# Kernel tuning notes

Hardware: AMD Instinct MI355X
Metric: run time of the kernel (lower is better)

## Reference

```python
import jax, jax.numpy as jnp
import numpy as np

N, D_IN, D_ATTN, STEPS, TOPK, TAU = 8192, 512, 64, 2, 16, 1.0
LN_EPS = 1e-5


def setup_inputs() -> dict:
    key = jax.random.key(0)
    ks = jax.random.split(key, 6)
    s_in = 1.0 / np.sqrt(D_IN)
    s_at = 1.0 / np.sqrt(D_ATTN)
    return {
        "X": jax.random.normal(ks[0], (N, D_IN), jnp.float32),
        "W1": jax.random.normal(ks[1], (D_ATTN, D_IN), jnp.float32) * s_in,
        "W2": jax.random.normal(ks[2], (D_ATTN, D_ATTN), jnp.float32) * s_at,
        "W3": jax.random.normal(ks[3], (D_ATTN, D_IN), jnp.float32) * s_in,
        "mixW": jax.random.normal(ks[4], (STEPS, D_IN, D_IN), jnp.float32) * s_in,
        "mixB": jax.random.normal(ks[5], (STEPS, D_IN), jnp.float32) * 0.01,
        "gamma": jnp.ones((D_IN,), jnp.float32),
        "beta": jnp.zeros((D_IN,), jnp.float32),
    }


def reference(X, W1, W2, W3, mixW, mixB, gamma, beta):
    # --- adjacency from features (top-k masked attention) ---
    Q = X @ W1.T                    # [N, d_attn]
    K = X @ W3.T                    # [N, d_attn]
    S = (Q @ W2) @ K.T / TAU        # [N, N]  (W2.weight used as raw matrix)
    _, idx = jax.lax.top_k(S, TOPK) # top-k along dim 1, [N, topk]
    mask = jnp.full_like(S, -jnp.inf)
    rows = jnp.arange(N)[:, None]
    mask = mask.at[rows, idx].set(0.0)
    P = jax.nn.softmax(S + mask, axis=1)  # row-sparse (k nonzeros) but dense-stored
    # dropout p=0 (eval mode) -> identity

    # --- iterative message passing with per-step mix ---
    H = X
    Z = jnp.zeros_like(X)
    for n in range(STEPS):  # bidir=False
        H = P @ H
        Z = Z + H @ mixW[n].T + mixB[n]

    # --- residual + LayerNorm ---
    y = X + Z
    mu = jnp.mean(y, axis=-1, keepdims=True)
    var = jnp.mean((y - mu) ** 2, axis=-1, keepdims=True)
    return (y - mu) * jax.lax.rsqrt(var + LN_EPS) * gamma + beta
```

## Files before the change

kernel.cpp:

```cpp
#include <hip/hip_runtime.h>

#define NROWS 8192
#define DIN   512
#define DATT  64
#define KTOP  16
#define CMAX  128
#define SROWS 32
#define NSPLIT 2
#define KSB   256
#define THRC  2.45f
#define NEG_INF (-3.0e38f)

typedef _Float16 f16x8 __attribute__((ext_vector_type(8)));
typedef float    fx4   __attribute__((ext_vector_type(4)));

__device__ __forceinline__ void gload_lds16(const void* g, void* l) {
    __builtin_amdgcn_global_load_lds((const __attribute__((address_space(1))) void*)g,
                                     (__attribute__((address_space(3))) void*)l, 16, 0, 0);
}

__global__ void k_conv_f16(const float* __restrict__ in, _Float16* __restrict__ out, int n) {
    int i = blockIdx.x * 256 + threadIdx.x;
    if (i < n) out[i] = (_Float16)in[i];
}

__global__ void k_split(const float* __restrict__ in, _Float16* __restrict__ hi,
                        _Float16* __restrict__ lo, int n) {
    int i = blockIdx.x * 256 + threadIdx.x;
    if (i < n) {
        float x = in[i];
        _Float16 h = (_Float16)x;
        hi[i] = h;
        lo[i] = (_Float16)(x - (float)h);
    }
}

__global__ void k_wsplit(const float* __restrict__ W1, const float* __restrict__ W2,
                         const float* __restrict__ W3, _Float16* __restrict__ Whi,
                         _Float16* __restrict__ Wlo, int* __restrict__ CandCnt) {
    int id = blockIdx.x * 256 + threadIdx.x;
    if (id < NROWS) CandCnt[id] = 0;
    int c = id >> 9, k = id & 511;
    float r;
    if (c < 64) {
        float acc = 0.f;
        #pragma unroll 8
        for (int e = 0; e < 64; e++) acc += W1[e*512 + k] * W2[e*64 + c];
        r = acc;
    } else {
        r = W3[(c - 64)*512 + k];
    }
    _Float16 h = (_Float16)r;
    Whi[id] = h;
    Wlo[id] = (_Float16)(r - (float)h);
}

__launch_bounds__(256)
__global__ void k_proj(const _Float16* __restrict__ Ahi, const _Float16* __restrict__ Alo,
                       const _Float16* __restrict__ Bhi, const _Float16* __restrict__ Blo,
                       float* __restrict__ Cf, _Float16* __restrict__ Ch) {
    const int tid = threadIdx.x, lane = tid & 63, wid = tid >> 6;
    const int bm = blockIdx.x * 128 + wid * 32;
    const int bn = blockIdx.y * 64;
    const int lr = lane & 15, kg = lane >> 4;

    fx4 acc[2][4];
    #pragma unroll
    for (int m = 0; m < 2; m++)
        #pragma unroll
        for (int n = 0; n < 4; n++) acc[m][n] = (fx4){0.f,0.f,0.f,0.f};

    const _Float16* Aph = Ahi + (size_t)(bm + lr) * DIN + kg*8;
    const _Float16* Apl = Alo + (size_t)(bm + lr) * DIN + kg*8;
    const _Float16* Bph = Bhi + (size_t)(bn + lr) * DIN + kg*8;
    const _Float16* Bpl = Blo + (size_t)(bn + lr) * DIN + kg*8;

    for (int k0 = 0; k0 < DIN; k0 += 32) {
        f16x8 ah[2], al[2], bh[4], bl[4];
        #pragma unroll
        for (int m = 0; m < 2; m++) {
            ah[m] = *(const f16x8*)(Aph + (size_t)m*16*DIN + k0);
            al[m] = *(const f16x8*)(Apl + (size_t)m*16*DIN + k0);
        }
        #pragma unroll
        for (int n = 0; n < 4; n++) {
            bh[n] = *(const f16x8*)(Bph + (size_t)n*16*DIN + k0);
            bl[n] = *(const f16x8*)(Bpl + (size_t)n*16*DIN + k0);
        }
        #pragma unroll
        for (int m = 0; m < 2; m++)
            #pragma unroll
            for (int n = 0; n < 4; n++) {
                acc[m][n] = __builtin_amdgcn_mfma_f32_16x16x32_f16(ah[m], bh[n], acc[m][n], 0,0,0);
                acc[m][n] = __builtin_amdgcn_mfma_f32_16x16x32_f16(ah[m], bl[n], acc[m][n], 0,0,0);
                acc[m][n] = __builtin_amdgcn_mfma_f32_16x16x32_f16(al[m], bh[n], acc[m][n], 0,0,0);
            }
    }

    #pragma unroll
    for (int m = 0; m < 2; m++)
        #pragma unroll
        for (int n = 0; n < 4; n++) {
            const int col = bn + n*16 + lr;
            #pragma unroll
            for (int r = 0; r < 4; r++) {
                const int row = bm + m*16 + kg*4 + r;
                const size_t off = (size_t)row * 128 + col;
                float v = acc[m][n][r];
                Cf[off] = v;
                Ch[off] = (_Float16)v;
            }
        }
}

__launch_bounds__(256)
__global__ void k_kstats1(const float* __restrict__ AK, float* __restrict__ KCp,
                          float* __restrict__ ksp) {
    __shared__ float kr[32][64];
    const int tid = threadIdx.x;
    const int r0  = blockIdx.x * 32;
    #pragma unroll
    for (int q = 0; q < 8; q++) {
        int e = tid + q*256;
        int rr = e >> 6, cc = e & 63;
        kr[rr][cc] = AK[(size_t)(r0 + rr) * 128 + 64 + cc];
    }
    __syncthreads();

    const int i0 = tid >> 2;
    const int j0 = (tid & 3) * 16;
    float acc[16];
    #pragma unroll
    for (int e = 0; e < 16; e++) acc[e] = 0.f;
    #pragma unroll 8
    for (int rr = 0; rr < 32; rr++) {
        const float ki = kr[rr][i0];
        #pragma unroll
        for (int e = 0; e < 16; e++) acc[e] += ki * kr[rr][j0 + e];
    }
    float* o = KCp + (size_t)blockIdx.x * 4096 + i0*64 + j0;
    #pragma unroll
    for (int e = 0; e < 16; e++) o[e] = acc[e];

    if (tid < 64) {
        float s = 0.f;
        #pragma unroll 8
        for (int rr = 0; rr < 32; rr++) s += kr[rr][tid];
        ksp[blockIdx.x*64 + tid] = s;
    }
}

__launch_bounds__(256)
__global__ void k_kstats2(const float* __restrict__ KCp, const float* __restrict__ ksp,
                          float* __restrict__ KC, float* __restrict__ ksum) {
    const int o = blockIdx.x*256 + threadIdx.x;
    float s0=0.f, s1=0.f, s2=0.f, s3=0.f;
    for (int b = 0; b < KSB; b += 4) {
        s0 += KCp[(size_t)b*4096 + o];
        s1 += KCp[(size_t)(b+1)*4096 + o];
        s2 += KCp[(size_t)(b+2)*4096 + o];
        s3 += KCp[(size_t)(b+3)*4096 + o];
    }
    KC[o] = (s0+s1) + (s2+s3);
    if (o < 64) {
        float t0=0.f, t1=0.f;
        for (int b = 0; b < KSB; b += 2) {
            t0 += ksp[b*64 + o];
            t1 += ksp[(b+1)*64 + o];
        }
        ksum[o] = t0 + t1;
    }
}

__launch_bounds__(256)
__global__ void k_thr(const float* __restrict__ AK, const float* __restrict__ ksum,
                      const float* __restrict__ KC, float* __restrict__ Thr) {
    __shared__ float sKC[64*65];
    __shared__ float skb[64];
    const int tid = threadIdx.x, lane = tid & 63, wv = tid >> 6;

    for (int e = tid; e < 4096; e += 256)
        sKC[(e >> 6)*65 + (e & 63)] = KC[e];
    if (tid < 64) skb[tid] = ksum[tid] * (1.f/(float)NROWS);
    __syncthreads();

    #pragma unroll
    for (int j = 0; j < 4; j++) {
        const int row = blockIdx.x*16 + wv*4 + j;
        const float a_l = AK[(size_t)row * 128 + lane];
        float w = 0.f;
        #pragma unroll 16
        for (int d = 0; d < 64; d++) w += sKC[lane*65 + d] * __shfl(a_l, d);
        float p  = a_l * w;
        float mu = a_l * skb[lane];
        #pragma unroll
        for (int off = 1; off < 64; off <<= 1) {
            p  += __shfl_xor(p,  off);
            mu += __shfl_xor(mu, off);
        }
        if (lane == 0) {
            float var = p * (1.f/(float)NROWS) - mu*mu;
            Thr[row] = mu + THRC * sqrtf(fmaxf(var, 0.f));
        }
    }
}

__launch_bounds__(256)
__global__ void k_sfilter(const _Float16* __restrict__ AKh, const float* __restrict__ Thr,
                          int* __restrict__ CandIdx, int* __restrict__ CandCnt) {
    const int tid = threadIdx.x, lane = tid & 63, wid = tid >> 6;
    const int bm = blockIdx.x * SROWS;
    const int lr = lane & 15, kg = lane >> 4;

    __shared__ int scnt[SROWS];
    __shared__ int sbase[SROWS];
    __shared__ int scand[SROWS][CMAX];
    if (tid < SROWS) scnt[tid] = 0;

    f16x8 af[2][2];
    #pragma unroll
    for (int m = 0; m < 2; m++)
        #pragma unroll
        for (int ks = 0; ks < 2; ks++)
            af[m][ks] = *(const f16x8*)(AKh + (size_t)(bm + m*16 + lr)*128 + ks*32 + kg*8);

    float thr[2][4];
    #pragma unroll
    for (int m = 0; m < 2; m++)
        #pragma unroll
        for (int r = 0; r < 4; r++)
            thr[m][r] = Thr[bm + m*16 + kg*4 + r];

    __syncthreads();

    const int c0 = blockIdx.y * (NROWS/NSPLIT) + wid*64;
    f16x8 bf[4][2], bnx[4][2];
    #pragma unroll
    for (int n = 0; n < 4; n++)
        #pragma unroll
        for (int ks = 0; ks < 2; ks++)
            bnx[n][ks] = *(const f16x8*)(AKh + (size_t)(c0 + n*16 + lr)*128 + 64 + ks*32 + kg*8);

    const int NIT = (NROWS/NSPLIT)/256;
    for (int it = 0; it < NIT; ++it) {
        #pragma unroll
        for (int n = 0; n < 4; n++)
            #pragma unroll
            for (int ks = 0; ks < 2; ks++)
                bf[n][ks] = bnx[n][ks];
        const int cbase = c0 + it*256;
        if (it + 1 < NIT) {
            const int cnx = cbase + 256;
            #pragma unroll
            for (int n = 0; n < 4; n++)
                #pragma unroll
                for (int ks = 0; ks < 2; ks++)
                    bnx[n][ks] = *(const f16x8*)(AKh + (size_t)(cnx + n*16 + lr)*128 + 64 + ks*32 + kg*8);
        }

        fx4 acc[2][4];
        #pragma unroll
        for (int m = 0; m < 2; m++)
            #pragma unroll
            for (int n = 0; n < 4; n++) acc[m][n] = (fx4){0.f,0.f,0.f,0.f};
        #pragma unroll
        for (int ks = 0; ks < 2; ks++)
            #pragma unroll
            for (int m = 0; m < 2; m++)
                #pragma unroll
                for (int n = 0; n < 4; n++)
                    acc[m][n] = __builtin_amdgcn_mfma_f32_16x16x32_f16(af[m][ks], bf[n][ks], acc[m][n], 0,0,0);

        #pragma unroll
        for (int m = 0; m < 2; m++) {
            #pragma unroll
            for (int r = 0; r < 4; r++) {
                const int row = m*16 + kg*4 + r;
                const float t = thr[m][r];
                #pragma unroll
                for (int n = 0; n < 4; n++) {
                    const float v = acc[m][n][r];
                    if (v > t) {
                        const int p = atomicAdd(&scnt[row], 1);
                        if (p < CMAX) scand[row][p] = cbase + n*16 + lr;
                    }
                }
            }
        }
    }

    __syncthreads();
    if (tid < SROWS) sbase[tid] = atomicAdd(&CandCnt[bm + tid], min(scnt[tid], CMAX));
    __syncthreads();
    for (int e = tid; e < SROWS*CMAX; e += 256) {
        const int row = e / CMAX, slot = e % CMAX;
        if (slot < min(scnt[row], CMAX)) {
            const int dst = sbase[row] + slot;
            if (dst < CMAX) CandIdx[(size_t)(bm + row)*CMAX + dst] = scand[row][slot];
        }
    }
}

__launch_bounds__(256)
__global__ void k_sel(const float* __restrict__ AK, const int* __restrict__ CandIdx,
                      const int* __restrict__ CandCnt,
                      float* __restrict__ Pval, int* __restrict__ Pidx) {
    const int wv   = threadIdx.x >> 6;
    const int row  = blockIdx.x*4 + wv;
    const int lane = threadIdx.x & 63;
    const int cnt  = min(CandCnt[row], CMAX);

    __shared__ float ss[4][CMAX];
    __shared__ int   sx[4][CMAX];

    const fx4* a4 = (const fx4*)(AK + (size_t)row * 128);

    float sv[2]; int si[2];
    #pragma unroll
    for (int q = 0; q < 2; q++) {
        const int c = lane + q*64;
        if (c < cnt) {
            const int idx = CandIdx[(size_t)row * CMAX + c];
            const fx4* k4 = (const fx4*)(AK + (size_t)idx * 128 + 64);
            float p0 = 0.f, p1 = 0.f, p2 = 0.f, p3 = 0.f;
            #pragma unroll
            for (int d = 0; d < 4; d++) {
                fx4 a0 = a4[d*4+0], k0 = k4[d*4+0];
                fx4 a1 = a4[d*4+1], k1 = k4[d*4+1];
                fx4 a2 = a4[d*4+2], k2 = k4[d*4+2];
                fx4 a3 = a4[d*4+3], k3 = k4[d*4+3];
                p0 += a0[0]*k0[0] + a0[1]*k0[1] + a0[2]*k0[2] + a0[3]*k0[3];
                p1 += a1[0]*k1[0] + a1[1]*k1[1] + a1[2]*k1[2] + a1[3]*k1[3];
                p2 += a2[0]*k2[0] + a2[1]*k2[1] + a2[2]*k2[2] + a2[3]*k2[3];
                p3 += a3[0]*k3[0] + a3[1]*k3[1] + a3[2]*k3[2] + a3[3]*k3[3];
            }
            sv[q] = (p0 + p1) + (p2 + p3); si[q] = idx;
        } else { sv[q] = NEG_INF; si[q] = 0x7fffffff; }
        ss[wv][c] = sv[q];
        sx[wv][c] = si[q];
    }

    float m = fmaxf(sv[0], sv[1]);
    #pragma unroll
    for (int off = 1; off < 64; off <<= 1) m = fmaxf(m, __shfl_xor(m, off));

    int r0 = 0, r1 = 0;
    #pragma unroll 4
    for (int j = 0; j < cnt; j++) {
        const float sj = ss[wv][j];
        const int   ij = sx[wv][j];
        r0 += (sj > sv[0]) || (sj == sv[0] && ij < si[0]);
        r1 += (sj > sv[1]) || (sj == sv[1] && ij < si[1]);
    }

    const float e0 = (lane      < cnt && r0 < KTOP) ? __expf(sv[0] - m) : 0.f;
    const float e1 = (lane + 64 < cnt && r1 < KTOP) ? __expf(sv[1] - m) : 0.f;
    float Z = e0 + e1;
    #pragma unroll
    for (int off = 1; off < 64; off <<= 1) Z += __shfl_xor(Z, off);
    const float rZ = 1.f / Z;

    if (lane < cnt && r0 < KTOP) {
        Pval[(size_t)row*KTOP + r0] = e0 * rZ;
        Pidx[(size_t)row*KTOP + r0] = si[0];
    }
    if (lane + 64 < cnt && r1 < KTOP) {
        Pval[(size_t)row*KTOP + r1] = e1 * rZ;
        Pidx[(size_t)row*KTOP + r1] = si[1];
    }
    if (lane >= cnt && lane < KTOP) {
        Pval[(size_t)row*KTOP + lane] = 0.f;
        Pidx[(size_t)row*KTOP + lane] = row;
    }
}

__launch_bounds__(256)
__global__ void k_gather(const float* __restrict__ Pval, const int* __restrict__ Pidx,
                         const _Float16* __restrict__ Hin, _Float16* __restrict__ Hout) {
    const int wv = threadIdx.x >> 6, lane = threadIdx.x & 63;
    const int row = blockIdx.x*4 + wv;
    const float pvl = Pval[row*KTOP + (lane & 15)];
    const int   pil = Pidx[row*KTOP + (lane & 15)];

    float acc[8];
    #pragma unroll
    for (int j = 0; j < 8; j++) acc[j] = 0.f;
    #pragma unroll
    for (int t = 0; t < KTOP; t++) {
        const float p  = __shfl(pvl, t);
        const int   ix = __shfl(pil, t);
        f16x8 h = *(const f16x8*)(Hin + (size_t)ix*DIN + lane*8);
        #pragma unroll
        for (int j = 0; j < 8; j++) acc[j] += p * (float)h[j];
    }
    f16x8 o;
    #pragma unroll
    for (int j = 0; j < 8; j++) o[j] = (_Float16)acc[j];
    *(f16x8*)(Hout + (size_t)row*DIN + lane*8) = o;
}

template<bool ACCUM>
__launch_bounds__(256)
__global__ void k_gemm_lds(const _Float16* __restrict__ A, const _Float16* __restrict__ B,
                           float* __restrict__ Cf, const float* __restrict__ bias,
                           int M, int N, int K) {
    __shared__ __align__(16) char smem[24576];
    const int tid = threadIdx.x, lane = tid & 63, wid = tid >> 6;
    const int bm = blockIdx.x * 128;
    const int bn = blockIdx.y * 64;
    const int lr = lane & 15, kg = lane >> 4;

    const int srow  = lane >> 3;
    const int scolh = ((lane & 7) ^ srow) * 8;

    fx4 acc[2][4];
    #pragma unroll
    for (int m = 0; m < 2; m++)
        #pragma unroll
        for (int n = 0; n < 4; n++) acc[m][n] = (fx4){0.f,0.f,0.f,0.f};

    const int sw = (lr & 7) << 4;

    for (int k0 = 0; k0 < K; k0 += 64) {
        #pragma unroll
        for (int q = 0; q < 4; q++) {
            const int r = (wid*4 + q)*8 + srow;
            gload_lds16(A + (size_t)(bm + r)*K + k0 + scolh, smem + (wid*4 + q)*1024);
        }
        #pragma unroll
        for (int q = 0; q < 2; q++) {
            const int r = (wid*2 + q)*8 + srow;
            gload_lds16(B + (size_t)(bn + r)*K + k0 + scolh, smem + 16384 + (wid*2 + q)*1024);
        }
        __syncthreads();

        f16x8 af[2][2], bf[4][2];
        #pragma unroll
        for (int m = 0; m < 2; m++) {
            const int arow = wid*32 + m*16 + lr;
            #pragma unroll
            for (int ks = 0; ks < 2; ks++)
                af[m][ks] = *(const f16x8*)(smem + arow*128 + ((ks*64 + kg*16) ^ sw));
        }
        #pragma unroll
        for (int n = 0; n < 4; n++) {
            const int brow = n*16 + lr;
            #pragma unroll
            for (int ks = 0; ks < 2; ks++)
                bf[n][ks] = *(const f16x8*)(smem + 16384 + brow*128 + ((ks*64 + kg*16) ^ sw));
        }
        #pragma unroll
        for (int ks = 0; ks < 2; ks++)
            #pragma unroll
            for (int m = 0; m < 2; m++)
                #pragma unroll
                for (int n = 0; n < 4; n++)
                    acc[m][n] = __builtin_amdgcn_mfma_f32_16x16x32_f16(af[m][ks], bf[n][ks], acc[m][n], 0,0,0);
        __syncthreads();
    }

    #pragma unroll
    for (int m = 0; m < 2; m++) {
        #pragma unroll
        for (int n = 0; n < 4; n++) {
            const int col = bn + n*16 + lr;
            const float bv = bias[col];
            #pragma unroll
            for (int r = 0; r < 4; r++) {
                const int row = bm + wid*32 + m*16 + kg*4 + r;
                const size_t off = (size_t)row * N + col;
                float v = acc[m][n][r] + bv;
                if (ACCUM) v += Cf[off];
                Cf[off] = v;
            }
        }
    }
}

__launch_bounds__(256)
__global__ void k_ln(const float* __restrict__ X, const float* __restrict__ Z,
                     const float* __restrict__ gamma, const float* __restrict__ beta,
                     float* __restrict__ out) {
    const int row = blockIdx.x, tid = threadIdx.x;
    const size_t base = (size_t)row * DIN;
    float y0 = X[base + tid]       + Z[base + tid];
    float y1 = X[base + tid + 256] + Z[base + tid + 256];
    float s  = y0 + y1;
    float s2 = y0*y0 + y1*y1;
    #pragma unroll
    for (int off = 32; off > 0; off >>= 1) {
        s  += __shfl_down(s,  off);
        s2 += __shfl_down(s2, off);
    }
    __shared__ float as_[4], as2_[4], mv[2];
    const int lane = tid & 63, w = tid >> 6;
    if (lane == 0) { as_[w] = s; as2_[w] = s2; }
    __syncthreads();
    if (tid == 0) {
        float ts = as_[0] + as_[1] + as_[2] + as_[3];
        float t2 = as2_[0] + as2_[1] + as2_[2] + as2_[3];
        float mu  = ts / 512.f;
        float var = t2 / 512.f - mu*mu;
        mv[0] = mu; mv[1] = rsqrtf(var + 1e-5f);
    }
    __syncthreads();
    const float mu = mv[0], rs = mv[1];
    out[base + tid]       = (y0 - mu) * rs * gamma[tid]       + beta[tid];
    out[base + tid + 256] = (y1 - mu) * rs * gamma[tid + 256] + beta[tid + 256];
}

extern "C" void kernel_launch(void* const* d_in, const int* in_sizes, int n_in,
                              void* d_out, int out_size, void* d_ws, size_t ws_size,
                              hipStream_t stream) {
    const float* X     = (const float*)d_in[0];
    const float* W1    = (const float*)d_in[1];
    const float* W2    = (const float*)d_in[2];
    const float* W3    = (const float*)d_in[3];
    const float* mixW  = (const float*)d_in[4];
    const float* mixB  = (const float*)d_in[5];
    const float* gamma = (const float*)d_in[6];
    const float* beta  = (const float*)d_in[7];
    float* out = (float*)d_out;

    char* ws = (char*)d_ws;
    size_t off = 0;
    auto alloc = [&](size_t bytes) {
        void* p = ws + off;
        off += (bytes + 255) & ~(size_t)255;
        return p;
    };
    _Float16* Xhi  = (_Float16*)alloc((size_t)NROWS*DIN*2);
    _Float16* Xlo  = (_Float16*)alloc((size_t)NROWS*DIN*2);
    _Float16* Whi  = (_Float16*)alloc((size_t)128*DIN*2);
    _Float16* Wlo  = (_Float16*)alloc((size_t)128*DIN*2);
    float*    Af32 = (float*)alloc((size_t)NROWS*128*4);
    _Float16* AKh  = (_Float16*)alloc((size_t)NROWS*128*2);
    _Float16* mWh  = (_Float16*)alloc((size_t)2*DIN*DIN*2);
    float*    KCp  = (float*)alloc((size_t)KSB*4096*4);
    float*    ksp  = (float*)alloc((size_t)KSB*64*4);
    float*    ksum = (float*)alloc(64*4);
    float*    KC   = (float*)alloc(4096*4);
    float*    Thr  = (float*)alloc((size_t)NROWS*4);
    float*    Pval = (float*)alloc((size_t)NROWS*KTOP*4);
    int*      Pidx = (int*)alloc((size_t)NROWS*KTOP*4);
    int*      CandIdx = (int*)alloc((size_t)NROWS*CMAX*4);
    int*      CandCnt = (int*)alloc((size_t)NROWS*4);
    _Float16* H1h  = (_Float16*)alloc((size_t)NROWS*DIN*2);
    _Float16* H2h  = (_Float16*)alloc((size_t)NROWS*DIN*2);
    float*    Zacc = (float*)alloc((size_t)NROWS*DIN*4);
    (void)ws_size; (void)in_sizes; (void)n_in; (void)out_size;

    dim3 b256(256);

    k_wsplit<<<dim3(128*DIN/256), b256, 0, stream>>>(W1, W2, W3, Whi, Wlo, CandCnt);
    k_split<<<dim3(NROWS*DIN/256), b256, 0, stream>>>(X, Xhi, Xlo, NROWS*DIN);
    k_conv_f16<<<dim3(2*DIN*DIN/256), b256, 0, stream>>>(mixW, mWh, 2*DIN*DIN);

    k_proj<<<dim3(NROWS/128, 2), b256, 0, stream>>>(Xhi, Xlo, Whi, Wlo, Af32, AKh);

    k_kstats1<<<dim3(KSB), b256, 0, stream>>>(Af32, KCp, ksp);
    k_kstats2<<<dim3(16), b256, 0, stream>>>(KCp, ksp, KC, ksum);
    k_thr<<<dim3(NROWS/16), b256, 0, stream>>>(Af32, ksum, KC, Thr);

    k_sfilter<<<dim3(NROWS/SROWS, NSPLIT), b256, 0, stream>>>(AKh, Thr, CandIdx, CandCnt);

    k_sel<<<dim3(NROWS/4), b256, 0, stream>>>(Af32, CandIdx, CandCnt, Pval, Pidx);

    k_gather<<<dim3(NROWS/4), b256, 0, stream>>>(Pval, Pidx, Xhi, H1h);
    k_gemm_lds<false><<<dim3(NROWS/128, DIN/64), b256, 0, stream>>>(
        H1h, mWh, Zacc, mixB, NROWS, DIN, DIN);
    k_gather<<<dim3(NROWS/4), b256, 0, stream>>>(Pval, Pidx, H1h, H2h);
    k_gemm_lds<true><<<dim3(NROWS/128, DIN/64), b256, 0, stream>>>(
        H2h, mWh + (size_t)DIN*DIN, Zacc, mixB + DIN, NROWS, DIN, DIN);
    k_ln<<<dim3(NROWS), b256, 0, stream>>>(X, Zacc, gamma, beta, out);
}
```

Baseline: 285.8 us.

## Fuse X hi/lo split into projection and merge two mix GEMMs into one K=1024 GEMM

Removes the standalone X split and mixW conversion kernels. The projection kernel now reads fp32 X directly, splits it into hi/lo f16 in registers, and writes Xhi from one column block. The two per-step mix GEMMs are concatenated along K into a single GEMM over [H1|H2] with a concatenated weight and summed bias. This avoids the Zacc read-modify-write and an extra launch. NSPLIT for the filter is also raised from 2 to 4; in exchange the projection does more fp32 global reads per block.

```diff
diff --git a/kernel.cpp b/kernel.cpp
--- a/kernel.cpp
+++ b/kernel.cpp
@@ -6,7 +6,7 @@
 #define KTOP  16
 #define CMAX  128
 #define SROWS 32
-#define NSPLIT 2
+#define NSPLIT 4
 #define KSB   256
 #define THRC  2.45f
 #define NEG_INF (-3.0e38f)
@@ -17,22 +17,6 @@
 __device__ __forceinline__ void gload_lds16(const void* g, void* l) {
     __builtin_amdgcn_global_load_lds((const __attribute__((address_space(1))) void*)g,
                                      (__attribute__((address_space(3))) void*)l, 16, 0, 0);
-}
-
-__global__ void k_conv_f16(const float* __restrict__ in, _Float16* __restrict__ out, int n) {
-    int i = blockIdx.x * 256 + threadIdx.x;
-    if (i < n) out[i] = (_Float16)in[i];
-}
-
-__global__ void k_split(const float* __restrict__ in, _Float16* __restrict__ hi,
-                        _Float16* __restrict__ lo, int n) {
-    int i = blockIdx.x * 256 + threadIdx.x;
-    if (i < n) {
-        float x = in[i];
-        _Float16 h = (_Float16)x;
-        hi[i] = h;
-        lo[i] = (_Float16)(x - (float)h);
-    }
 }
 
 __global__ void k_wsplit(const float* __restrict__ W1, const float* __restrict__ W2,
@@ -55,14 +39,24 @@
     Wlo[id] = (_Float16)(r - (float)h);
 }
 
-__launch_bounds__(256)
-__global__ void k_proj(const _Float16* __restrict__ Ahi, const _Float16* __restrict__ Alo,
-                       const _Float16* __restrict__ Bhi, const _Float16* __restrict__ Blo,
-                       float* __restrict__ Cf, _Float16* __restrict__ Ch) {
+__global__ void k_mixprep(const float* __restrict__ mixW, const float* __restrict__ mixB,
+                          _Float16* __restrict__ mWcat, float* __restrict__ biasSum) {
+    int id = blockIdx.x * 256 + threadIdx.x;
+    int j = id >> 10, k = id & 1023;
+    float v = (k < 512) ? mixW[j*512 + k] : mixW[262144 + j*512 + (k - 512)];
+    mWcat[id] = (_Float16)v;
+    if (id < 512) biasSum[id] = mixB[id] + mixB[512 + id];
+}
+
+__launch_bounds__(256)
+__global__ void k_proj(const float* __restrict__ X, const _Float16* __restrict__ Bhi,
+                       const _Float16* __restrict__ Blo, float* __restrict__ Cf,
+                       _Float16* __restrict__ Ch, _Float16* __restrict__ Xhi) {
     const int tid = threadIdx.x, lane = tid & 63, wid = tid >> 6;
     const int bm = blockIdx.x * 128 + wid * 32;
     const int bn = blockIdx.y * 64;
     const int lr = lane & 15, kg = lane >> 4;
+    const bool wx = (blockIdx.y == 0);
 
     fx4 acc[2][4];
     #pragma unroll
@@ -70,8 +64,6 @@
         #pragma unroll
         for (int n = 0; n < 4; n++) acc[m][n] = (fx4){0.f,0.f,0.f,0.f};
 
-    const _Float16* Aph = Ahi + (size_t)(bm + lr) * DIN + kg*8;
-    const _Float16* Apl = Alo + (size_t)(bm + lr) * DIN + kg*8;
     const _Float16* Bph = Bhi + (size_t)(bn + lr) * DIN + kg*8;
     const _Float16* Bpl = Blo + (size_t)(bn + lr) * DIN + kg*8;
 
@@ -79,8 +71,16 @@
         f16x8 ah[2], al[2], bh[4], bl[4];
         #pragma unroll
         for (int m = 0; m < 2; m++) {
-            ah[m] = *(const f16x8*)(Aph + (size_t)m*16*DIN + k0);
-            al[m] = *(const f16x8*)(Apl + (size_t)m*16*DIN + k0);
+            const fx4* xp = (const fx4*)(X + (size_t)(bm + m*16 + lr)*DIN + kg*8 + k0);
+            fx4 x0 = xp[0], x1 = xp[1];
+            #pragma unroll
+            for (int j = 0; j < 4; j++) {
+                _Float16 h0 = (_Float16)x0[j];
+                _Float16 h1 = (_Float16)x1[j];
+                ah[m][j]   = h0; al[m][j]   = (_Float16)(x0[j] - (float)h0);
+                ah[m][j+4] = h1; al[m][j+4] = (_Float16)(x1[j] - (float)h1);
+            }
+            if (wx) *(f16x8*)(Xhi + (size_t)(bm + m*16 + lr)*DIN + kg*8 + k0) = ah[m];
         }
         #pragma unroll
         for (int n = 0; n < 4; n++) {
@@ -399,11 +399,10 @@
     *(f16x8*)(Hout + (size_t)row*DIN + lane*8) = o;
 }
 
-template<bool ACCUM>
-__launch_bounds__(256)
-__global__ void k_gemm_lds(const _Float16* __restrict__ A, const _Float16* __restrict__ B,
-                           float* __restrict__ Cf, const float* __restrict__ bias,
-                           int M, int N, int K) {
+__launch_bounds__(256)
+__global__ void k_gemm_mix(const _Float16* __restrict__ A1, const _Float16* __restrict__ A2,
+                           const _Float16* __restrict__ B, float* __restrict__ Cf,
+                           const float* __restrict__ bias) {
     __shared__ __align__(16) char smem[24576];
     const int tid = threadIdx.x, lane = tid & 63, wid = tid >> 6;
     const int bm = blockIdx.x * 128;
@@ -421,16 +420,18 @@
 
     const int sw = (lr & 7) << 4;
 
-    for (int k0 = 0; k0 < K; k0 += 64) {
+    for (int k0 = 0; k0 < 1024; k0 += 64) {
+        const _Float16* Asrc = (k0 < 512) ? A1 : A2;
+        const int ka = k0 & 511;
         #pragma unroll
         for (int q = 0; q < 4; q++) {
             const int r = (wid*4 + q)*8 + srow;
-            gload_lds16(A + (size_t)(bm + r)*K + k0 + scolh, smem + (wid*4 + q)*1024);
+            gload_lds16(Asrc + (size_t)(bm + r)*DIN + ka + scolh, smem + (wid*4 + q)*1024);
         }
         #pragma unroll
         for (int q = 0; q < 2; q++) {
             const int r = (wid*2 + q)*8 + srow;
-            gload_lds16(B + (size_t)(bn + r)*K + k0 + scolh, smem + 16384 + (wid*2 + q)*1024);
+            gload_lds16(B + (size_t)(bn + r)*1024 + k0 + scolh, smem + 16384 + (wid*2 + q)*1024);
         }
         __syncthreads();
 
@@ -468,10 +469,7 @@
             #pragma unroll
             for (int r = 0; r < 4; r++) {
                 const int row = bm + wid*32 + m*16 + kg*4 + r;
-                const size_t off = (size_t)row * N + col;
-                float v = acc[m][n][r] + bv;
-                if (ACCUM) v += Cf[off];
-                Cf[off] = v;
+                Cf[(size_t)row * DIN + col] = acc[m][n][r] + bv;
             }
         }
     }
@@ -530,12 +528,12 @@
         return p;
     };
     _Float16* Xhi  = (_Float16*)alloc((size_t)NROWS*DIN*2);
-    _Float16* Xlo  = (_Float16*)alloc((size_t)NROWS*DIN*2);
     _Float16* Whi  = (_Float16*)alloc((size_t)128*DIN*2);
     _Float16* Wlo  = (_Float16*)alloc((size_t)128*DIN*2);
     float*    Af32 = (float*)alloc((size_t)NROWS*128*4);
     _Float16* AKh  = (_Float16*)alloc((size_t)NROWS*128*2);
-    _Float16* mWh  = (_Float16*)alloc((size_t)2*DIN*DIN*2);
+    _Float16* mWcat= (_Float16*)alloc((size_t)DIN*1024*2);
+    float*    bSum = (float*)alloc(512*4);
     float*    KCp  = (float*)alloc((size_t)KSB*4096*4);
     float*    ksp  = (float*)alloc((size_t)KSB*64*4);
     float*    ksum = (float*)alloc(64*4);
@@ -553,10 +551,9 @@
     dim3 b256(256);
 
     k_wsplit<<<dim3(128*DIN/256), b256, 0, stream>>>(W1, W2, W3, Whi, Wlo, CandCnt);
-    k_split<<<dim3(NROWS*DIN/256), b256, 0, stream>>>(X, Xhi, Xlo, NROWS*DIN);
-    k_conv_f16<<<dim3(2*DIN*DIN/256), b256, 0, stream>>>(mixW, mWh, 2*DIN*DIN);
-
-    k_proj<<<dim3(NROWS/128, 2), b256, 0, stream>>>(Xhi, Xlo, Whi, Wlo, Af32, AKh);
+    k_mixprep<<<dim3(DIN*1024/256), b256, 0, stream>>>(mixW, mixB, mWcat, bSum);
+
+    k_proj<<<dim3(NROWS/128, 2), b256, 0, stream>>>(X, Whi, Wlo, Af32, AKh, Xhi);
 
     k_kstats1<<<dim3(KSB), b256, 0, stream>>>(Af32, KCp, ksp);
     k_kstats2<<<dim3(16), b256, 0, stream>>>(KCp, ksp, KC, ksum);
@@ -567,10 +564,9 @@
     k_sel<<<dim3(NROWS/4), b256, 0, stream>>>(Af32, CandIdx, CandCnt, Pval, Pidx);
 
     k_gather<<<dim3(NROWS/4), b256, 0, stream>>>(Pval, Pidx, Xhi, H1h);
-    k_gemm_lds<false><<<dim3(NROWS/128, DIN/64), b256, 0, stream>>>(
-        H1h, mWh, Zacc, mixB, NROWS, DIN, DIN);
     k_gather<<<dim3(NROWS/4), b256, 0, stream>>>(Pval, Pidx, H1h, H2h);
-    k_gemm_lds<true><<<dim3(NROWS/128, DIN/64), b256, 0, stream>>>(
-        H2h, mWh + (size_t)DIN*DIN, Zacc, mixB + DIN, NROWS, DIN, DIN);
+
+    k_gemm_mix<<<dim3(NROWS/128, DIN/64), b256, 0, stream>>>(H1h, H2h, mWcat, Zacc, bSum);
+
     k_ln<<<dim3(NROWS), b256, 0, stream>>>(X, Zacc, gamma, beta, out);
 }
```

Result: faster. 274.8 us (-3.8%).
